# Kernel tuning notes

Measured on AMD Instinct MI355X. Metric: run time of the kernel, lower is better.

Reference implementation:

```python
import jax, jax.numpy as jnp
import numpy as np

B, S = 2, 4096
H, D = 8, 64      # num_heads, per-head embed_dim
W = 128           # window (even)
O = 64            # num_outputs per head
ZERO_VALUE = 0.0


def setup_inputs() -> dict:
    key = jax.random.key(0)
    kq, kk, kv, kwq, kwk, kbq, kbk, ko = jax.random.split(key, 8)
    scale = 1.0 / np.sqrt(D)
    return {
        "q": jax.random.normal(kq, (B, S, H * D), dtype=jnp.float32),
        "k": jax.random.normal(kk, (B, S, H * D), dtype=jnp.float32),
        "v": jax.random.normal(kv, (B, S, H * O), dtype=jnp.float32),
        "Wq": jax.random.normal(kwq, (D, D), dtype=jnp.float32) * scale,
        "bq": jax.random.normal(kbq, (D,), dtype=jnp.float32) * 0.02,
        "Wk": jax.random.normal(kwk, (D, D), dtype=jnp.float32) * scale,
        "bk": jax.random.normal(kbk, (D,), dtype=jnp.float32) * 0.02,
        "ocpe": jax.random.normal(ko, (W + 1, H), dtype=jnp.float32) * 0.02,
    }


def reference(q, k, v, Wq, bq, Wk, bk, ocpe):
    b, s, _ = q.shape
    p = W // 2
    assert s % W == 0
    C = s // W  # number of chunks of size `window`

    # split heads + per-head projections (nn.Linear: x @ W.T + b)
    q = q.reshape(b, s, H, D) @ Wq.T + bq
    k = k.reshape(b, s, H, D) @ Wk.T + bk
    v = v.reshape(b, s, H, O)

    # pad seq dim by window//2 on both sides (matches F.pad in source)
    qp = jnp.pad(q, ((0, 0), (p, p), (0, 0), (0, 0)))
    kp = jnp.pad(k, ((0, 0), (p, p), (0, 0), (0, 0)))
    vp = jnp.pad(v, ((0, 0), (p, p), (0, 0), (0, 0)))

    # overlapping chunks of length 2W (chunk_size=W plus 2*p halo)
    starts = jnp.arange(C) * W                 # (C,)
    loc = jnp.arange(2 * W)                    # (2W,)
    idx = starts[:, None] + loc[None, :]       # (C, 2W) indices into padded seq
    qc = qp[:, idx]                            # (B, C, 2W, H, D)
    kc = kp[:, idx]
    vc = vp[:, idx]                            # (B, C, 2W, H, O)

    scores = jnp.einsum('ncxhd,ncyhd->ncxyh', qc, kc)  # (B,C,2W,2W,H)

    diff = loc[None, :] - loc[:, None]         # j - i, (2W, 2W)
    within = jnp.abs(diff) <= p                # (2W, 2W)
    bias = jnp.where(within[:, :, None],
                     ocpe[jnp.clip(p + diff, 0, W)], 0.0)  # (2W,2W,H)
    scores = scores + bias[None, None]

    # boundary mask: global padded position must lie in [p, s+p)
    pos = starts[:, None] + loc[None, :]       # (C, 2W)
    valid = (pos >= p) & (pos < s + p)         # (C, 2W)
    mask = within[None] & valid[:, :, None] & valid[:, None, :]  # (C,2W,2W)

    scores = jnp.where(mask[None, :, :, :, None], scores, ZERO_VALUE)
    attn = jnp.tanh(scores)

    res = jnp.einsum('ncxyh,ncyhd->ncxd', attn, vc)  # (B,C,2W,O)
    out = res[:, :, p:2 * W - p].reshape(b, s, O)     # middle W rows per chunk

    # attn_flat[b,c,i,d,h] = attn[b,c, i+p, i+d, h]
    r = jnp.arange(W)
    rows = r[:, None] + p                      # (W, 1)
    cols = r[:, None] + jnp.arange(W + 1)[None]  # (W, W+1)
    attn_flat = attn[:, :, rows, cols, :]      # (B, C, W, W+1, H)
    attn_flat = attn_flat.reshape(b, s, W + 1, H)
    return attn_flat, out
```

## Files before the change

kernel.cpp:

```cpp
#include <hip/hip_runtime.h>
#include <cstddef>

#define SB 2
#define SS 4096
#define SH 8
#define SD 64
#define SP 64
#define SNO 129
#define TQ 16
#define WN 144
#define NT16 (SS/TQ)
#define SSTR 168

typedef _Float16 f16;
typedef __attribute__((ext_vector_type(8))) _Float16 f16x8;
typedef __attribute__((ext_vector_type(4))) float floatx4;

union f16frag { f16 h[8]; ushort4 u4[2]; f16x8 v; };

__device__ __forceinline__ float fast_tanh(float x) {
  float ax = fabsf(x);
  float e = __expf(2.0f * ax);
  float t = 1.0f - 2.0f / (e + 1.0f);
  return copysignf(t, x);
}

__device__ __forceinline__ void cvt16(const float* __restrict__ src, f16* __restrict__ dst) {
  float4 x0 = *(const float4*)(src);
  float4 x1 = *(const float4*)(src + 4);
  float4 x2 = *(const float4*)(src + 8);
  float4 x3 = *(const float4*)(src + 12);
  f16frag a, c;
  a.h[0]=(f16)x0.x; a.h[1]=(f16)x0.y; a.h[2]=(f16)x0.z; a.h[3]=(f16)x0.w;
  a.h[4]=(f16)x1.x; a.h[5]=(f16)x1.y; a.h[6]=(f16)x1.z; a.h[7]=(f16)x1.w;
  c.h[0]=(f16)x2.x; c.h[1]=(f16)x2.y; c.h[2]=(f16)x2.z; c.h[3]=(f16)x2.w;
  c.h[4]=(f16)x3.x; c.h[5]=(f16)x3.y; c.h[6]=(f16)x3.z; c.h[7]=(f16)x3.w;
  *(ushort4*)(dst)      = a.u4[0];
  *(ushort4*)(dst + 4)  = a.u4[1];
  *(ushort4*)(dst + 8)  = c.u4[0];
  *(ushort4*)(dst + 12) = c.u4[1];
}

__global__ __launch_bounds__(256) void prep_kernel(
    const float* __restrict__ q, const float* __restrict__ k, const float* __restrict__ v,
    const float* __restrict__ Wq, const float* __restrict__ bq,
    const float* __restrict__ Wk, const float* __restrict__ bk,
    f16* __restrict__ Qf, f16* __restrict__ Kf, f16* __restrict__ Vt)
{
  __shared__ f16 sWq[64*72], sWk[64*72], sQr[64*72], sKr[64*72], sVr[64*72];
  __shared__ float sbq[64], sbk[64];

  int t = threadIdx.x;
  int blk = blockIdx.x;
  int c = blk & 63; int bh = blk >> 6; int h = bh & 7; int b = bh >> 3;
  int s0 = c * 64;

  int dr = t >> 2, e0 = (t & 3) * 16;
  cvt16(Wq + dr*64 + e0, &sWq[dr*72 + e0]);
  cvt16(Wk + dr*64 + e0, &sWk[dr*72 + e0]);
  {
    size_t rbase = ((size_t)(b*SS + s0 + dr)) * (SH*SD) + h*SD + e0;
    cvt16(q + rbase, &sQr[dr*72 + e0]);
    cvt16(k + rbase, &sKr[dr*72 + e0]);
    cvt16(v + rbase, &sVr[dr*72 + e0]);
  }
  if (t < 64) { sbq[t] = bq[t]; sbk[t] = bk[t]; }
  __syncthreads();

  int lane = t & 63, wave = t >> 6;
  int r16 = lane & 15, g = lane >> 4;

  size_t hsbase = (size_t)(b*SH + h) * SS;

  #pragma unroll
  for (int j = 0; j < 4; ++j) {
    int tt = wave + 4*j;
    int si = tt >> 2, dj = tt & 3;
    floatx4 accq = {0.f,0.f,0.f,0.f}, acck = {0.f,0.f,0.f,0.f};
    #pragma unroll
    for (int e = 0; e < 64; e += 32) {
      f16x8 aq = *(const f16x8*)&sQr[(si*16 + r16)*72 + e + g*8];
      f16x8 ak = *(const f16x8*)&sKr[(si*16 + r16)*72 + e + g*8];
      f16x8 wq8 = *(const f16x8*)&sWq[(dj*16 + r16)*72 + e + g*8];
      f16x8 wk8 = *(const f16x8*)&sWk[(dj*16 + r16)*72 + e + g*8];
      accq = __builtin_amdgcn_mfma_f32_16x16x32_f16(aq, wq8, accq, 0, 0, 0);
      acck = __builtin_amdgcn_mfma_f32_16x16x32_f16(ak, wk8, acck, 0, 0, 0);
    }
    float biasq = sbq[dj*16 + r16];
    float biask = sbk[dj*16 + r16];
    #pragma unroll
    for (int rr = 0; rr < 4; ++rr) {
      int srow = s0 + si*16 + g*4 + rr;
      Qf[(hsbase + srow)*64 + dj*16 + r16] = (f16)(accq[rr] + biasq);
      Kf[(hsbase + srow)*64 + dj*16 + r16] = (f16)(acck[rr] + biask);
    }
  }

  {
    int d = t >> 2, p4 = t & 3, sc0 = p4 * 16;
    f16frag a, c2;
    #pragma unroll
    for (int j2 = 0; j2 < 8; ++j2) a.h[j2] = sVr[(sc0 + j2)*72 + d];
    #pragma unroll
    for (int j2 = 0; j2 < 8; ++j2) c2.h[j2] = sVr[(sc0 + 8 + j2)*72 + d];
    f16* dst = Vt + ((size_t)(b*SH + h)*64 + d)*SS + s0 + sc0;
    *(ushort4*)dst       = a.u4[0];
    *(ushort4*)(dst + 4) = a.u4[1];
    *(ushort4*)(dst + 8) = c2.u4[0];
    *(ushort4*)(dst + 12)= c2.u4[1];
  }
}

__global__ __launch_bounds__(512, 4) void attn_fused(
    const f16* __restrict__ Qf, const f16* __restrict__ Kf, const f16* __restrict__ Vt,
    const float* __restrict__ ocpe, float* __restrict__ af, float* __restrict__ outp)
{
  __shared__ f16 sPriv[SH][TQ*SSTR];
  __shared__ f16 sAF[TQ*SNO*SH];
  __shared__ float sObT[SH*SNO];

  int t = threadIdx.x;
  int lane = t & 63, wave = t >> 6;
  int r16 = lane & 15, g = lane >> 4;

  int blk = blockIdx.x;
  int G = (blk & 7) * 64 + (blk >> 3);
  int b = G >> 8, t16 = G & 255;
  int t0 = t16 * TQ, yg0 = t0 - SP;

  int h = wave;
  const f16* qb = Qf + ((size_t)(b*SH + h)*SS + t0 + r16)*64;
  f16x8 qa0 = *(const f16x8*)(qb + g*8);
  f16x8 qa1 = *(const f16x8*)(qb + 32 + g*8);

  for (int idx = t; idx < SNO*SH; idx += 512) {
    int o = idx >> 3, h2 = idx & 7;
    sObT[h2*SNO + o] = ocpe[idx];
  }

  f16* priv = &sPriv[wave][0];
  #pragma unroll
  for (int j = 0; j < 4; ++j)
    priv[r16*SSTR + WN + g*4 + j] = (f16)0.f;

  __syncthreads();

  const float* ob = &sObT[h*SNO];
  const f16* kbase = Kf + ((size_t)(b*SH + h)*SS)*64;
  floatx4 acc2[4] = {{0.f,0.f,0.f,0.f},{0.f,0.f,0.f,0.f},{0.f,0.f,0.f,0.f},{0.f,0.f,0.f,0.f}};

  bool interior = (t16 >= 4) & (t16 <= 250);

  if (interior) {
    const f16* krow = kbase + (size_t)(yg0 + r16) * 64 + g*8;
    #pragma unroll
    for (int yy = 0; yy < 9; ++yy) {
      f16x8 kb0 = *(const f16x8*)(krow + yy*1024);
      f16x8 kb1 = *(const f16x8*)(krow + yy*1024 + 32);
      floatx4 acc = {0.f,0.f,0.f,0.f};
      acc = __builtin_amdgcn_mfma_f32_16x16x32_f16(qa0, kb0, acc, 0, 0, 0);
      acc = __builtin_amdgcn_mfma_f32_16x16x32_f16(qa1, kb1, acc, 0, 0, 0);
      int y = yy*16 + r16;
      #pragma unroll
      for (int rr = 0; rr < 4; ++rr) {
        int i = g*4 + rr;
        int o = y - i;
        bool ook = (o >= 0) & (o <= 2*SP);
        float a = 0.f;
        if (ook) a = fast_tanh(acc[rr] + ob[o]);
        priv[i*SSTR + y] = (f16)a;
        if (ook) sAF[((size_t)i*SNO + o)*SH + h] = (f16)a;
      }
    }
    const f16* vrow = Vt + ((size_t)(b*SH + h)*64 + r16)*SS + yg0 + g*8;
    #pragma unroll
    for (int ks = 0; ks < 5; ++ks) {
      int yb = ks*32 + g*8;
      f16x8 a0 = *(const f16x8*)&priv[r16*SSTR + yb];
      #pragma unroll
      for (int dq = 0; dq < 4; ++dq) {
        f16x8 bv = *(const f16x8*)(vrow + (size_t)(dq*16)*SS + ks*32);
        acc2[dq] = __builtin_amdgcn_mfma_f32_16x16x32_f16(a0, bv, acc2[dq], 0, 0, 0);
      }
    }
  } else {
    #pragma unroll
    for (int yy = 0; yy < 9; ++yy) {
      int y = yy*16 + r16;
      int ygr = yg0 + y;
      int ygc = min(max(ygr, 0), SS-1);
      bool yok = (ygr >= 0) & (ygr < SS);
      const f16* kr = kbase + (size_t)ygc * 64;
      f16x8 kb0 = *(const f16x8*)(kr + g*8);
      f16x8 kb1 = *(const f16x8*)(kr + 32 + g*8);
      floatx4 acc = {0.f,0.f,0.f,0.f};
      acc = __builtin_amdgcn_mfma_f32_16x16x32_f16(qa0, kb0, acc, 0, 0, 0);
      acc = __builtin_amdgcn_mfma_f32_16x16x32_f16(qa1, kb1, acc, 0, 0, 0);
      #pragma unroll
      for (int rr = 0; rr < 4; ++rr) {
        int i = g*4 + rr;
        int o = y - i;
        bool ook = (o >= 0) & (o <= 2*SP);
        float a = 0.f;
        if (yok & ook) a = fast_tanh(acc[rr] + ob[o]);
        priv[i*SSTR + y] = (f16)a;
        if (ook) sAF[((size_t)i*SNO + o)*SH + h] = (f16)a;
      }
    }
    const f16* vb0 = Vt + ((size_t)(b*SH + h)*64 + r16)*SS;
    #pragma unroll
    for (int ks = 0; ks < 5; ++ks) {
      int yb = ks*32 + g*8;
      int ygr = yg0 + yb;
      int ygc = min(max(ygr, 0), SS-8);
      f16x8 a0 = *(const f16x8*)&priv[r16*SSTR + yb];
      #pragma unroll
      for (int dq = 0; dq < 4; ++dq) {
        f16x8 bv = *(const f16x8*)(vb0 + (size_t)(dq*16)*SS + ygc);
        acc2[dq] = __builtin_amdgcn_mfma_f32_16x16x32_f16(a0, bv, acc2[dq], 0, 0, 0);
      }
    }
  }

  {
    float* po = (float*)priv;
    #pragma unroll
    for (int dq = 0; dq < 4; ++dq)
      #pragma unroll
      for (int rr = 0; rr < 4; ++rr)
        po[(g*4 + rr)*64 + dq*16 + r16] = acc2[dq][rr];
  }

  __syncthreads();

  {
    int e2 = t * 2;
    int i = e2 >> 6, d = e2 & 63;
    float sx = 0.f, sy = 0.f;
    #pragma unroll
    for (int h2 = 0; h2 < SH; ++h2) {
      const float* ph = (const float*)&sPriv[h2][0];
      sx += ph[i*64 + d];
      sy += ph[i*64 + d + 1];
    }
    *(float2*)(outp + ((size_t)b*SS + t0 + i)*64 + d) = make_float2(sx, sy);
  }

  {
    float* afb = af + ((size_t)b*SS + t0) * (size_t)(SNO*SH);
    for (int idx = t; idx < TQ*SNO*SH/4; idx += 512) {
      const f16* s = &sAF[idx*4];
      float4 w = make_float4((float)s[0], (float)s[1], (float)s[2], (float)s[3]);
      *(float4*)(afb + idx*4) = w;
    }
  }
}

extern "C" void kernel_launch(void* const* d_in, const int* in_sizes, int n_in,
                              void* d_out, int out_size, void* d_ws, size_t ws_size,
                              hipStream_t stream) {
  const float* q    = (const float*)d_in[0];
  const float* k    = (const float*)d_in[1];
  const float* v    = (const float*)d_in[2];
  const float* Wq   = (const float*)d_in[3];
  const float* bq   = (const float*)d_in[4];
  const float* Wk   = (const float*)d_in[5];
  const float* bk   = (const float*)d_in[6];
  const float* ocpe = (const float*)d_in[7];

  f16* Kf = (f16*)d_ws;
  f16* Vt = Kf + (size_t)SB*SH*SS*SD;
  f16* Qf = Vt + (size_t)SB*SH*SS*SD;

  float* af = (float*)d_out;
  float* op = af + (size_t)SB*SS*SNO*SH;

  prep_kernel<<<SB*SH*64, 256, 0, stream>>>(q, k, v, Wq, bq, Wk, bk, Qf, Kf, Vt);
  attn_fused<<<SB*NT16, 512, 0, stream>>>(Qf, Kf, Vt, ocpe, af, op);
}
```

Measured before the change: 44.59 us.

## Fuse Q projection into attention kernel and add MFMA priority hints

Moves the Q projection out of the prep kernel into the attention kernel. Each wave now loads its raw fp32 q rows, converts them to fp16 and multiplies them by Wq (staged in shared memory) with MFMA, so the fp16 Qf buffer is never written to or read back from global memory. It also wraps MFMA sequences in s_setprio to raise wave priority during matrix work. The cost is more shared memory and extra prologue work in the attention kernel, which could lower occupancy there.

```diff
diff --git a/kernel.cpp b/kernel.cpp
--- a/kernel.cpp
+++ b/kernel.cpp
@@ -42,13 +42,12 @@
 }
 
 __global__ __launch_bounds__(256) void prep_kernel(
-    const float* __restrict__ q, const float* __restrict__ k, const float* __restrict__ v,
-    const float* __restrict__ Wq, const float* __restrict__ bq,
+    const float* __restrict__ k, const float* __restrict__ v,
     const float* __restrict__ Wk, const float* __restrict__ bk,
-    f16* __restrict__ Qf, f16* __restrict__ Kf, f16* __restrict__ Vt)
+    f16* __restrict__ Kf, f16* __restrict__ Vt)
 {
-  __shared__ f16 sWq[64*72], sWk[64*72], sQr[64*72], sKr[64*72], sVr[64*72];
-  __shared__ float sbq[64], sbk[64];
+  __shared__ f16 sWk[64*72], sKr[64*72], sVr[64*72];
+  __shared__ float sbk[64];
 
   int t = threadIdx.x;
   int blk = blockIdx.x;
@@ -56,15 +55,13 @@
   int s0 = c * 64;
 
   int dr = t >> 2, e0 = (t & 3) * 16;
-  cvt16(Wq + dr*64 + e0, &sWq[dr*72 + e0]);
   cvt16(Wk + dr*64 + e0, &sWk[dr*72 + e0]);
   {
     size_t rbase = ((size_t)(b*SS + s0 + dr)) * (SH*SD) + h*SD + e0;
-    cvt16(q + rbase, &sQr[dr*72 + e0]);
     cvt16(k + rbase, &sKr[dr*72 + e0]);
     cvt16(v + rbase, &sVr[dr*72 + e0]);
   }
-  if (t < 64) { sbq[t] = bq[t]; sbk[t] = bk[t]; }
+  if (t < 64) sbk[t] = bk[t];
   __syncthreads();
 
   int lane = t & 63, wave = t >> 6;
@@ -76,22 +73,17 @@
   for (int j = 0; j < 4; ++j) {
     int tt = wave + 4*j;
     int si = tt >> 2, dj = tt & 3;
-    floatx4 accq = {0.f,0.f,0.f,0.f}, acck = {0.f,0.f,0.f,0.f};
+    floatx4 acck = {0.f,0.f,0.f,0.f};
     #pragma unroll
     for (int e = 0; e < 64; e += 32) {
-      f16x8 aq = *(const f16x8*)&sQr[(si*16 + r16)*72 + e + g*8];
       f16x8 ak = *(const f16x8*)&sKr[(si*16 + r16)*72 + e + g*8];
-      f16x8 wq8 = *(const f16x8*)&sWq[(dj*16 + r16)*72 + e + g*8];
       f16x8 wk8 = *(const f16x8*)&sWk[(dj*16 + r16)*72 + e + g*8];
-      accq = __builtin_amdgcn_mfma_f32_16x16x32_f16(aq, wq8, accq, 0, 0, 0);
       acck = __builtin_amdgcn_mfma_f32_16x16x32_f16(ak, wk8, acck, 0, 0, 0);
     }
-    float biasq = sbq[dj*16 + r16];
     float biask = sbk[dj*16 + r16];
     #pragma unroll
     for (int rr = 0; rr < 4; ++rr) {
       int srow = s0 + si*16 + g*4 + rr;
-      Qf[(hsbase + srow)*64 + dj*16 + r16] = (f16)(accq[rr] + biasq);
       Kf[(hsbase + srow)*64 + dj*16 + r16] = (f16)(acck[rr] + biask);
     }
   }
@@ -112,12 +104,16 @@
 }
 
 __global__ __launch_bounds__(512, 4) void attn_fused(
-    const f16* __restrict__ Qf, const f16* __restrict__ Kf, const f16* __restrict__ Vt,
+    const float* __restrict__ q,  const float* __restrict__ Wq, const float* __restrict__ bq,
+    const f16* __restrict__ Kf, const f16* __restrict__ Vt,
     const float* __restrict__ ocpe, float* __restrict__ af, float* __restrict__ outp)
 {
   __shared__ f16 sPriv[SH][TQ*SSTR];
   __shared__ f16 sAF[TQ*SNO*SH];
+  __shared__ f16 sWq[64*72];
+  __shared__ f16 sQp[SH][TQ*72];
   __shared__ float sObT[SH*SNO];
+  __shared__ float sBq[64];
 
   int t = threadIdx.x;
   int lane = t & 63, wave = t >> 6;
@@ -129,10 +125,18 @@
   int t0 = t16 * TQ, yg0 = t0 - SP;
 
   int h = wave;
-  const f16* qb = Qf + ((size_t)(b*SH + h)*SS + t0 + r16)*64;
-  f16x8 qa0 = *(const f16x8*)(qb + g*8);
-  f16x8 qa1 = *(const f16x8*)(qb + 32 + g*8);
-
+
+  {
+    int dr = t >> 3, e8 = (t & 7) * 8;
+    float4 w0 = *(const float4*)(Wq + dr*64 + e8);
+    float4 w1 = *(const float4*)(Wq + dr*64 + e8 + 4);
+    f16frag fw;
+    fw.h[0]=(f16)w0.x; fw.h[1]=(f16)w0.y; fw.h[2]=(f16)w0.z; fw.h[3]=(f16)w0.w;
+    fw.h[4]=(f16)w1.x; fw.h[5]=(f16)w1.y; fw.h[6]=(f16)w1.z; fw.h[7]=(f16)w1.w;
+    *(ushort4*)&sWq[dr*72 + e8]     = fw.u4[0];
+    *(ushort4*)&sWq[dr*72 + e8 + 4] = fw.u4[1];
+    if (t < 64) sBq[t] = bq[t];
+  }
   for (int idx = t; idx < SNO*SH; idx += 512) {
     int o = idx >> 3, h2 = idx & 7;
     sObT[h2*SNO + o] = ocpe[idx];
@@ -145,6 +149,37 @@
 
   __syncthreads();
 
+  {
+    const float* qraw = q + (((size_t)(b*SS + t0 + r16))*SH + h)*SD;
+    float4 a0 = *(const float4*)(qraw + g*8);
+    float4 a1 = *(const float4*)(qraw + g*8 + 4);
+    float4 a2 = *(const float4*)(qraw + 32 + g*8);
+    float4 a3 = *(const float4*)(qraw + 32 + g*8 + 4);
+    f16frag fa, fb;
+    fa.h[0]=(f16)a0.x; fa.h[1]=(f16)a0.y; fa.h[2]=(f16)a0.z; fa.h[3]=(f16)a0.w;
+    fa.h[4]=(f16)a1.x; fa.h[5]=(f16)a1.y; fa.h[6]=(f16)a1.z; fa.h[7]=(f16)a1.w;
+    fb.h[0]=(f16)a2.x; fb.h[1]=(f16)a2.y; fb.h[2]=(f16)a2.z; fb.h[3]=(f16)a2.w;
+    fb.h[4]=(f16)a3.x; fb.h[5]=(f16)a3.y; fb.h[6]=(f16)a3.z; fb.h[7]=(f16)a3.w;
+    f16x8 aq0 = fa.v, aq1 = fb.v;
+    f16* qp = &sQp[h][0];
+    #pragma unroll
+    for (int dj = 0; dj < 4; ++dj) {
+      f16x8 b0 = *(const f16x8*)&sWq[(dj*16 + r16)*72 + g*8];
+      f16x8 b1 = *(const f16x8*)&sWq[(dj*16 + r16)*72 + 32 + g*8];
+      floatx4 acc = {0.f,0.f,0.f,0.f};
+      __builtin_amdgcn_s_setprio(1);
+      acc = __builtin_amdgcn_mfma_f32_16x16x32_f16(aq0, b0, acc, 0, 0, 0);
+      acc = __builtin_amdgcn_mfma_f32_16x16x32_f16(aq1, b1, acc, 0, 0, 0);
+      __builtin_amdgcn_s_setprio(0);
+      float bias = sBq[dj*16 + r16];
+      #pragma unroll
+      for (int rr = 0; rr < 4; ++rr)
+        qp[(g*4 + rr)*72 + dj*16 + r16] = (f16)(acc[rr] + bias);
+    }
+  }
+  f16x8 qa0 = *(const f16x8*)&sQp[h][r16*72 + g*8];
+  f16x8 qa1 = *(const f16x8*)&sQp[h][r16*72 + 32 + g*8];
+
   const float* ob = &sObT[h*SNO];
   const f16* kbase = Kf + ((size_t)(b*SH + h)*SS)*64;
   floatx4 acc2[4] = {{0.f,0.f,0.f,0.f},{0.f,0.f,0.f,0.f},{0.f,0.f,0.f,0.f},{0.f,0.f,0.f,0.f}};
@@ -158,8 +193,10 @@
       f16x8 kb0 = *(const f16x8*)(krow + yy*1024);
       f16x8 kb1 = *(const f16x8*)(krow + yy*1024 + 32);
       floatx4 acc = {0.f,0.f,0.f,0.f};
+      __builtin_amdgcn_s_setprio(1);
       acc = __builtin_amdgcn_mfma_f32_16x16x32_f16(qa0, kb0, acc, 0, 0, 0);
       acc = __builtin_amdgcn_mfma_f32_16x16x32_f16(qa1, kb1, acc, 0, 0, 0);
+      __builtin_amdgcn_s_setprio(0);
       int y = yy*16 + r16;
       #pragma unroll
       for (int rr = 0; rr < 4; ++rr) {
@@ -177,11 +214,13 @@
     for (int ks = 0; ks < 5; ++ks) {
       int yb = ks*32 + g*8;
       f16x8 a0 = *(const f16x8*)&priv[r16*SSTR + yb];
+      __builtin_amdgcn_s_setprio(1);
       #pragma unroll
       for (int dq = 0; dq < 4; ++dq) {
         f16x8 bv = *(const f16x8*)(vrow + (size_t)(dq*16)*SS + ks*32);
         acc2[dq] = __builtin_amdgcn_mfma_f32_16x16x32_f16(a0, bv, acc2[dq], 0, 0, 0);
       }
+      __builtin_amdgcn_s_setprio(0);
     }
   } else {
     #pragma unroll
@@ -270,11 +309,10 @@
 
   f16* Kf = (f16*)d_ws;
   f16* Vt = Kf + (size_t)SB*SH*SS*SD;
-  f16* Qf = Vt + (size_t)SB*SH*SS*SD;
 
   float* af = (float*)d_out;
   float* op = af + (size_t)SB*SS*SNO*SH;
 
-  prep_kernel<<<SB*SH*64, 256, 0, stream>>>(q, k, v, Wq, bq, Wk, bk, Qf, Kf, Vt);
-  attn_fused<<<SB*NT16, 512, 0, stream>>>(Qf, Kf, Vt, ocpe, af, op);
-}
+  prep_kernel<<<SB*SH*64, 256, 0, stream>>>(k, v, Wk, bk, Kf, Vt);
+  attn_fused<<<SB*NT16, 512, 0, stream>>>(q, Wq, bq, Kf, Vt, ocpe, af, op);
+}
```

Result: no change. 45.44 us (+1.9%).
